# Kernel tuning notes

Measured on AMD Instinct MI355X. Metric: run time of the kernel, lower is better.

Reference implementation:

```python
import jax, jax.numpy as jnp
import numpy as np

N_NODES = 65536
N_EDGES = N_NODES * 16
NEG_SLOPE = 0.2


def setup_inputs() -> dict:
    key = jax.random.key(0)
    ks = jax.random.split(key, 32)
    x = jax.random.normal(ks[0], (N_NODES, 336), dtype=jnp.float32)
    ei = jax.random.randint(ks[1], (2, N_EDGES), 0, N_NODES)
    src, dst = ei[0], ei[1]
    dst = jnp.where(src == dst, (dst + 1) % N_NODES, dst)  # no pre-existing self-loops
    edge_index = jnp.stack([src, dst])
    batch = jnp.arange(N_NODES) // 8

    def mk(k, shape, fan_in):
        return jax.random.normal(k, shape, dtype=jnp.float32) * (1.0 / np.sqrt(fan_in))

    conv_dims = [(336, 125), (250, 75), (150, 50), (100, 30)]
    H = 2
    p = {}
    ki = 2
    for i, (cin, cout) in enumerate(conv_dims, 1):
        p[f"W{i}"] = mk(ks[ki], (cin, H * cout), cin); ki += 1
        p[f"as{i}"] = mk(ks[ki], (H, cout), cout); ki += 1
        p[f"ad{i}"] = mk(ks[ki], (H, cout), cout); ki += 1
        p[f"b{i}"] = jnp.zeros((H * cout,), dtype=jnp.float32)
    lin_dims = [(480, 200), (200, 100), (100, 100), (100, 29)]
    for i, (cin, cout) in enumerate(lin_dims, 1):
        p[f"lw{i}"] = mk(ks[ki], (cin, cout), cin); ki += 1
        p[f"lb{i}"] = jnp.zeros((cout,), dtype=jnp.float32)
    return {"x": x, "edge_index": edge_index, "batch": batch, **p}


def gat_conv(x, src, dst, W, a_src, a_dst, bias):
    # PyG GATConv (concat=True): gather -> LeakyReLU score -> segment softmax over dst -> scatter-add
    N = x.shape[0]
    H, C = a_src.shape
    h = (x @ W).reshape(N, H, C)                      # [N,H,C]
    al_s = jnp.sum(h * a_src, axis=-1)                # [N,H]
    al_d = jnp.sum(h * a_dst, axis=-1)
    e = jax.nn.leaky_relu(al_s[src] + al_d[dst], NEG_SLOPE)  # [E,H]
    m = jax.ops.segment_max(e, dst, num_segments=N)   # [N,H]
    m = jnp.where(jnp.isfinite(m), m, 0.0)
    ex = jnp.exp(e - m[dst])
    den = jax.ops.segment_sum(ex, dst, num_segments=N)
    alpha = ex / den[dst]                             # [E,H]
    out = jax.ops.segment_sum(alpha[:, :, None] * h[src], dst, num_segments=N)
    return out.reshape(N, H * C) + bias


def reference(x, edge_index, batch,
              W1, as1, ad1, b1, W2, as2, ad2, b2,
              W3, as3, ad3, b3, W4, as4, ad4, b4,
              lw1, lb1, lw2, lb2, lw3, lb3, lw4, lb4):
    N = x.shape[0]
    loops = jnp.arange(N)
    src = jnp.concatenate([edge_index[0], loops])  # add self-loops (PyG default)
    dst = jnp.concatenate([edge_index[1], loops])
    h = jax.nn.relu(gat_conv(x, src, dst, W1, as1, ad1, b1))
    h = jax.nn.relu(gat_conv(h, src, dst, W2, as2, ad2, b2))
    h = jax.nn.relu(gat_conv(h, src, dst, W3, as3, ad3, b3))
    h = jax.nn.relu(gat_conv(h, src, dst, W4, as4, ad4, b4))
    h = h.reshape(-1, 480)                         # 8 nodes per graph * 60 feats
    h = jax.nn.relu(h @ lw1 + lb1)
    h = jax.nn.relu(h @ lw2 + lb2)
    h = jax.nn.relu(h @ lw3 + lb3)
    return h @ lw4 + lb4
```

## Files before the change

### kernel.cpp

```cpp
#include <hip/hip_runtime.h>
#include <hip/hip_bf16.h>
#include <stdint.h>

#define N_NODES 65536
#define N_EDGES (N_NODES * 16)
#define NEG_SLOPE 0.2f

typedef short bf16x8 __attribute__((ext_vector_type(8)));
typedef float f32x4 __attribute__((ext_vector_type(4)));

__device__ __forceinline__ unsigned short f2bf(float f) {
    unsigned u = __float_as_uint(f);
    u += 0x7fffu + ((u >> 16) & 1u);
    return (unsigned short)(u >> 16);
}
__device__ __forceinline__ float bf2f(unsigned short h) {
    return __uint_as_float(((unsigned)h) << 16);
}
__device__ __forceinline__ void load_lds16(const void* g, void* l) {
    __builtin_amdgcn_global_load_lds(
        (const __attribute__((address_space(1))) unsigned int*)g,
        (__attribute__((address_space(3))) unsigned int*)l, 16, 0, 0);
}

template<int TN>
__global__ __launch_bounds__(256) void gemm_mfma(
    const float* __restrict__ A32, int KA,
    const unsigned short* __restrict__ Ahi, const unsigned short* __restrict__ Alo,
    int lda, int Kp,
    const unsigned short* __restrict__ Bhi, const unsigned short* __restrict__ Blo,
    const float* __restrict__ bias, int Nbias,
    float* __restrict__ C32,
    unsigned short* __restrict__ Chi, unsigned short* __restrict__ Clo,
    int ldc, int Nw, int relu,
    const float* __restrict__ asrc, const float* __restrict__ adst,
    float* __restrict__ alS, float* __restrict__ alD, int Cal, int HCal)
{
    constexpr int NI = TN / 32;
    __shared__ unsigned short sAhi[128 * 32], sAlo[128 * 32];
    __shared__ unsigned short sBhi[TN * 32],  sBlo[TN * 32];
    __shared__ float sAl[128][2][4];
    const int tid = threadIdx.x;
    const int wave = tid >> 6, lane = tid & 63;
    const int row0 = blockIdx.y * 128;
    const int col0 = blockIdx.x * TN;
    const int wm = (wave & 1) * 64, wn = (wave >> 1) * (TN / 2);
    const int mlane = lane & 15, q = lane >> 4;

    f32x4 acc[4][NI];
#pragma unroll
    for (int a = 0; a < 4; ++a)
#pragma unroll
        for (int b = 0; b < NI; ++b) acc[a][b] = (f32x4){0.f, 0.f, 0.f, 0.f};

    for (int k0 = 0; k0 < Kp; k0 += 32) {
        __syncthreads();
        if (A32) {
            const int r = tid >> 1, cbase = (tid & 1) * 16;
            const float* Ap = A32 + (size_t)(row0 + r) * lda;
#pragma unroll
            for (int j = 0; j < 4; ++j) {
                int kc = k0 + cbase + j * 4;
                float4 v = make_float4(0.f, 0.f, 0.f, 0.f);
                if (kc < KA) v = *(const float4*)(Ap + kc);
                ushort4 h, l;
                h.x = f2bf(v.x); l.x = f2bf(v.x - bf2f(h.x));
                h.y = f2bf(v.y); l.y = f2bf(v.y - bf2f(h.y));
                h.z = f2bf(v.z); l.z = f2bf(v.z - bf2f(h.z));
                h.w = f2bf(v.w); l.w = f2bf(v.w - bf2f(h.w));
                *(ushort4*)(sAhi + r * 32 + cbase + j * 4) = h;
                *(ushort4*)(sAlo + r * 32 + cbase + j * 4) = l;
            }
        } else {
#pragma unroll
            for (int cc = 0; cc < 2; ++cc) {
                int c = wave * 2 + cc;
                int r = c * 16 + (lane >> 2);
                size_t goff = (size_t)(row0 + r) * lda + k0 + (lane & 3) * 8;
                load_lds16(Ahi + goff, sAhi + c * 512);
                load_lds16(Alo + goff, sAlo + c * 512);
            }
        }
        {
#pragma unroll
            for (int cc = 0; cc < TN / 64; ++cc) {
                int c = wave * (TN / 64) + cc;
                int r = c * 16 + (lane >> 2);
                size_t goff = (size_t)(col0 + r) * Kp + k0 + (lane & 3) * 8;
                load_lds16(Bhi + goff, sBhi + c * 512);
                load_lds16(Blo + goff, sBlo + c * 512);
            }
        }
        __syncthreads();

        bf16x8 ah[4], al[4], bh[NI], bl[NI];
#pragma unroll
        for (int mi = 0; mi < 4; ++mi) {
            int m = wm + mi * 16 + mlane;
            ah[mi] = *(const bf16x8*)(sAhi + m * 32 + q * 8);
            al[mi] = *(const bf16x8*)(sAlo + m * 32 + q * 8);
        }
#pragma unroll
        for (int ni = 0; ni < NI; ++ni) {
            int n = wn + ni * 16 + mlane;
            bh[ni] = *(const bf16x8*)(sBhi + n * 32 + q * 8);
            bl[ni] = *(const bf16x8*)(sBlo + n * 32 + q * 8);
        }
#pragma unroll
        for (int mi = 0; mi < 4; ++mi)
#pragma unroll
            for (int ni = 0; ni < NI; ++ni) {
                acc[mi][ni] = __builtin_amdgcn_mfma_f32_16x16x32_bf16(ah[mi], bh[ni], acc[mi][ni], 0, 0, 0);
                acc[mi][ni] = __builtin_amdgcn_mfma_f32_16x16x32_bf16(al[mi], bh[ni], acc[mi][ni], 0, 0, 0);
                acc[mi][ni] = __builtin_amdgcn_mfma_f32_16x16x32_bf16(ah[mi], bl[ni], acc[mi][ni], 0, 0, 0);
            }
    }

#pragma unroll
    for (int ni = 0; ni < NI; ++ni) {
        int col = col0 + wn + ni * 16 + mlane;
        if (col >= Nw) continue;
        float bv = (bias && col < Nbias) ? bias[col] : 0.f;
#pragma unroll
        for (int mi = 0; mi < 4; ++mi) {
#pragma unroll
            for (int reg = 0; reg < 4; ++reg) {
                int row = row0 + wm + mi * 16 + q * 4 + reg;
                float v = acc[mi][ni][reg] + bv;
                if (relu) v = fmaxf(v, 0.f);
                size_t off = (size_t)row * ldc + col;
                if (Chi) {
                    unsigned short h = f2bf(v);
                    Chi[off] = h;
                    Clo[off] = f2bf(v - bf2f(h));
                } else {
                    C32[off] = v;
                }
            }
        }
    }

    if (asrc) {
        float asv[NI], adv[NI];
        bool head0[NI];
#pragma unroll
        for (int ni = 0; ni < NI; ++ni) {
            int col = col0 + wn + ni * 16 + mlane;
            bool valid = col < HCal;
            head0[ni] = col < Cal;
            asv[ni] = valid ? asrc[col] : 0.f;
            adv[ni] = valid ? adst[col] : 0.f;
        }
#pragma unroll
        for (int mi = 0; mi < 4; ++mi) {
#pragma unroll
            for (int reg = 0; reg < 4; ++reg) {
                float s0 = 0.f, s1 = 0.f, d0 = 0.f, d1 = 0.f;
#pragma unroll
                for (int ni = 0; ni < NI; ++ni) {
                    float v = acc[mi][ni][reg];
                    if (head0[ni]) { s0 += v * asv[ni]; d0 += v * adv[ni]; }
                    else           { s1 += v * asv[ni]; d1 += v * adv[ni]; }
                }
#pragma unroll
                for (int off = 1; off < 16; off <<= 1) {
                    s0 += __shfl_xor(s0, off); s1 += __shfl_xor(s1, off);
                    d0 += __shfl_xor(d0, off); d1 += __shfl_xor(d1, off);
                }
                if (mlane == 0) {
                    int rl = wm + mi * 16 + q * 4 + reg;
                    int slot = wave >> 1;
                    sAl[rl][slot][0] = s0; sAl[rl][slot][1] = s1;
                    sAl[rl][slot][2] = d0; sAl[rl][slot][3] = d1;
                }
            }
        }
        __syncthreads();
        if (tid < 128) {
            int row = row0 + tid;
            float v0 = sAl[tid][0][0] + sAl[tid][1][0];
            float v1 = sAl[tid][0][1] + sAl[tid][1][1];
            float v2 = sAl[tid][0][2] + sAl[tid][1][2];
            float v3 = sAl[tid][0][3] + sAl[tid][1][3];
            atomicAdd(&alS[row * 2 + 0], v0);
            atomicAdd(&alS[row * 2 + 1], v1);
            atomicAdd(&alD[row * 2 + 0], v2);
            atomicAdd(&alD[row * 2 + 1], v3);
        }
    }
}

template<int NI>
__device__ __forceinline__ void mlp_layer(
    const unsigned short* aHi, const unsigned short* aLo, int ldaS, int K,
    const unsigned short* __restrict__ Bhi, const unsigned short* __restrict__ Blo,
    int Kp,
    unsigned short* sBh, unsigned short* sBl,
    const float* __restrict__ bias, int Nbias, int colBase,
    unsigned short* oHi, unsigned short* oLo, int ldo, int Nstore,
    float* __restrict__ gOut, int row0, int relu,
    int wave, int lane)
{
    const int mlane = lane & 15, q = lane >> 4;
    const int wm = (wave & 1) * 16;
    const int wn = (wave >> 1) * (NI * 16);
    f32x4 acc[NI];
#pragma unroll
    for (int b = 0; b < NI; ++b) acc[b] = (f32x4){0.f, 0.f, 0.f, 0.f};

    for (int k0 = 0; k0 < K; k0 += 32) {
        __syncthreads();
        for (int c = wave; c < NI * 2; c += 4) {
            int r = c * 16 + (lane >> 2);
            size_t goff = (size_t)r * Kp + k0 + (lane & 3) * 8;
            load_lds16(Bhi + goff, sBh + c * 512);
            load_lds16(Blo + goff, sBl + c * 512);
        }
        __syncthreads();

        bf16x8 ah, al, bh[NI], bl[NI];
        ah = *(const bf16x8*)(aHi + (wm + mlane) * ldaS + k0 + q * 8);
        al = *(const bf16x8*)(aLo + (wm + mlane) * ldaS + k0 + q * 8);
#pragma unroll
        for (int ni = 0; ni < NI; ++ni) {
            int n = wn + ni * 16 + mlane;
            bh[ni] = *(const bf16x8*)(sBh + n * 32 + q * 8);
            bl[ni] = *(const bf16x8*)(sBl + n * 32 + q * 8);
        }
#pragma unroll
        for (int ni = 0; ni < NI; ++ni) {
            acc[ni] = __builtin_amdgcn_mfma_f32_16x16x32_bf16(ah, bh[ni], acc[ni], 0, 0, 0);
            acc[ni] = __builtin_amdgcn_mfma_f32_16x16x32_bf16(al, bh[ni], acc[ni], 0, 0, 0);
            acc[ni] = __builtin_amdgcn_mfma_f32_16x16x32_bf16(ah, bl[ni], acc[ni], 0, 0, 0);
        }
    }
    __syncthreads();

#pragma unroll
    for (int ni = 0; ni < NI; ++ni) {
        int colg = colBase + wn + ni * 16 + mlane;
        float bv = (colg < Nbias) ? bias[colg] : 0.f;
#pragma unroll
        for (int reg = 0; reg < 4; ++reg) {
            int row = wm + q * 4 + reg;
            float v = acc[ni][reg] + bv;
            if (relu) v = fmaxf(v, 0.f);
            if (gOut) {
                if (colg < 29) gOut[(size_t)(row0 + row) * 29 + colg] = v;
            } else if (colg < Nstore) {
                unsigned short h = f2bf(v);
                oHi[row * ldo + colg] = h;
                oLo[row * ldo + colg] = f2bf(v - bf2f(h));
            }
        }
    }
}

__global__ __launch_bounds__(256) void mlp_fused(
    const unsigned short* __restrict__ actHi, const unsigned short* __restrict__ actLo,
    const unsigned short* __restrict__ L1h, const unsigned short* __restrict__ L1l,
    const unsigned short* __restrict__ L2h, const unsigned short* __restrict__ L2l,
    const unsigned short* __restrict__ L3h, const unsigned short* __restrict__ L3l,
    const unsigned short* __restrict__ L4h, const unsigned short* __restrict__ L4l,
    const float* __restrict__ B1, const float* __restrict__ B2,
    const float* __restrict__ B3, const float* __restrict__ B4,
    float* __restrict__ out)
{
    __shared__ unsigned short b1h[32 * 224], b1l[32 * 224];
    __shared__ unsigned short b2h[32 * 128], b2l[32 * 128];
    __shared__ unsigned short sAh[32 * 32],  sAl[32 * 32];
    __shared__ unsigned short sBh[128 * 32], sBl[128 * 32];
    const int tid = threadIdx.x;
    const int wave = tid >> 6, lane = tid & 63;
    const int row0 = blockIdx.x * 32;
    const int mlane = lane & 15, q = lane >> 4;
    const int wm = (wave & 1) * 16;
    const int wn = (wave >> 1) * 64;

    for (int nt = 0; nt < 2; ++nt) {
        const unsigned short* Bh = L1h + (size_t)nt * 128 * 512;
        const unsigned short* Bl = L1l + (size_t)nt * 128 * 512;
        f32x4 acc[4];
#pragma unroll
        for (int b = 0; b < 4; ++b) acc[b] = (f32x4){0.f, 0.f, 0.f, 0.f};
        for (int k0 = 0; k0 < 512; k0 += 32) {
            __syncthreads();
            for (int c = wave; c < 2; c += 4) {
                int r = c * 16 + (lane >> 2);
                size_t goff = (size_t)(row0 + r) * 512 + k0 + (lane & 3) * 8;
                load_lds16(actHi + goff, sAh + c * 512);
                load_lds16(actLo + goff, sAl + c * 512);
            }
            for (int c = wave; c < 8; c += 4) {
                int r = c * 16 + (lane >> 2);
                size_t goff = (size_t)r * 512 + k0 + (lane & 3) * 8;
                load_lds16(Bh + goff, sBh + c * 512);
                load_lds16(Bl + goff, sBl + c * 512);
            }
            __syncthreads();
            bf16x8 ah = *(const bf16x8*)(sAh + (wm + mlane) * 32 + q * 8);
            bf16x8 al = *(const bf16x8*)(sAl + (wm + mlane) * 32 + q * 8);
#pragma unroll
            for (int ni = 0; ni < 4; ++ni) {
                int n = wn + ni * 16 + mlane;
                bf16x8 bh = *(const bf16x8*)(sBh + n * 32 + q * 8);
                bf16x8 bl = *(const bf16x8*)(sBl + n * 32 + q * 8);
                acc[ni] = __builtin_amdgcn_mfma_f32_16x16x32_bf16(ah, bh, acc[ni], 0, 0, 0);
                acc[ni] = __builtin_amdgcn_mfma_f32_16x16x32_bf16(al, bh, acc[ni], 0, 0, 0);
                acc[ni] = __builtin_amdgcn_mfma_f32_16x16x32_bf16(ah, bl, acc[ni], 0, 0, 0);
            }
        }
        __syncthreads();
#pragma unroll
        for (int ni = 0; ni < 4; ++ni) {
            int colg = nt * 128 + wn + ni * 16 + mlane;
            float bv = (colg < 200) ? B1[colg] : 0.f;
#pragma unroll
            for (int reg = 0; reg < 4; ++reg) {
                int row = wm + q * 4 + reg;
                float v = fmaxf(acc[ni][reg] + bv, 0.f);
                if (colg < 224) {
                    unsigned short h = f2bf(v);
                    b1h[row * 224 + colg] = h;
                    b1l[row * 224 + colg] = f2bf(v - bf2f(h));
                }
            }
        }
    }
    __syncthreads();

    mlp_layer<4>(b1h, b1l, 224, 224, L2h, L2l, 224, sBh, sBl,
                 B2, 100, 0, b2h, b2l, 128, 128, nullptr, 0, 1, wave, lane);
    __syncthreads();
    mlp_layer<4>(b2h, b2l, 128, 128, L3h, L3l, 128, sBh, sBl,
                 B3, 100, 0, b1h, b1l, 128, 128, nullptr, 0, 1, wave, lane);
    __syncthreads();
    mlp_layer<2>(b1h, b1l, 128, 128, L4h, L4l, 128, sBh, sBl,
                 B4, 29, 0, nullptr, nullptr, 0, 0, out, row0, 0, wave, lane);
}

struct WtJob {
    const float* W; unsigned short* Whi; unsigned short* Wlo;
    int K, N, Kp, remap, nb0;
};
struct WtJobs { WtJob j[8]; };

__global__ void wt_decomp_all(WtJobs jobs)
{
    int b = blockIdx.x;
    int idx = 0;
#pragma unroll
    for (int i = 1; i < 8; ++i)
        if (b >= jobs.j[i].nb0) idx = i;
    WtJob jb = jobs.j[idx];
    int n = b - jb.nb0;
    for (int k = threadIdx.x; k < jb.Kp; k += 256) {
        int ks = k, valid = 1;
        if (jb.remap) {
            int bb = k >> 6, r = k & 63;
            if (r < 60) ks = bb * 60 + r; else valid = 0;
        }
        float v = 0.f;
        if (valid && ks < jb.K && n < jb.N) v = jb.W[(size_t)ks * jb.N + n];
        unsigned short h = f2bf(v);
        jb.Whi[(size_t)n * jb.Kp + k] = h;
        jb.Wlo[(size_t)n * jb.Kp + k] = f2bf(v - bf2f(h));
    }
}

template<int LPE>
__global__ __launch_bounds__(256) void gat_gather_fused(
    const float* __restrict__ hlin,
    const float* __restrict__ al_s, const float* __restrict__ al_d,
    const int* __restrict__ indptr, const int* __restrict__ csr_src,
    const float* __restrict__ bias,
    unsigned short* __restrict__ outHi, unsigned short* __restrict__ outLo,
    int ldo, int Nn, int C, int HC, int HCpad)
{
    constexpr int G = 64 / LPE;
    const int wave = threadIdx.x >> 6, lane = threadIdx.x & 63;
    const int i = blockIdx.x * 4 + wave;
    if (i >= Nn) return;
    const int start = indptr[i], end = indptr[i + 1];
    const float ad0 = al_d[2 * i], ad1 = al_d[2 * i + 1];

    float m0 = -1e30f, m1 = -1e30f, den0 = 0.f, den1 = 0.f;
    for (int j = start + lane; j < end; j += 64) {
        int s = csr_src[j];
        float2 as = *(const float2*)(al_s + 2 * s);
        float e0 = as.x + ad0; e0 = e0 > 0.f ? e0 : NEG_SLOPE * e0;
        float e1 = as.y + ad1; e1 = e1 > 0.f ? e1 : NEG_SLOPE * e1;
        float n0 = fmaxf(m0, e0);
        den0 = den0 * __expf(m0 - n0) + __expf(e0 - n0);
        m0 = n0;
        float n1 = fmaxf(m1, e1);
        den1 = den1 * __expf(m1 - n1) + __expf(e1 - n1);
        m1 = n1;
    }
#pragma unroll
    for (int off = 32; off; off >>= 1) {
        float mo0 = __shfl_xor(m0, off), do0 = __shfl_xor(den0, off);
        float n0 = fmaxf(m0, mo0);
        den0 = den0 * __expf(m0 - n0) + do0 * __expf(mo0 - n0);
        m0 = n0;
        float mo1 = __shfl_xor(m1, off), do1 = __shfl_xor(den1, off);
        float n1 = fmaxf(m1, mo1);
        den1 = den1 * __expf(m1 - n1) + do1 * __expf(mo1 - n1);
        m1 = n1;
    }
    const float inv0 = 1.f / den0, inv1 = 1.f / den1;

    const int l = lane % LPE;
    const int g = lane / LPE;
    const int ch4 = l * 4;
    const bool chA = ch4 < HCpad;
    float a0 = 0.f, a1 = 0.f, a2 = 0.f, a3 = 0.f;
    const bool h0 = (ch4 + 0) < C, h1 = (ch4 + 1) < C,
               h2 = (ch4 + 2) < C, h3 = (ch4 + 3) < C;

    for (int jb = start; jb < end; jb += 4 * G) {
#pragma unroll
        for (int u = 0; u < 4; ++u) {
            int j = jb + u * G + g;
            int jj = j < end ? j : end - 1;
            int s = csr_src[jj];
            float2 as = *(const float2*)(al_s + 2 * s);
            float e0 = as.x + ad0; e0 = e0 > 0.f ? e0 : NEG_SLOPE * e0;
            float e1 = as.y + ad1; e1 = e1 > 0.f ? e1 : NEG_SLOPE * e1;
            float w0 = __expf(e0 - m0) * inv0;
            float w1 = __expf(e1 - m1) * inv1;
            if (j >= end) { w0 = 0.f; w1 = 0.f; }
            const float* hr = hlin + (size_t)s * HCpad;
            float4 h = chA ? *(const float4*)(hr + ch4)
                           : make_float4(0.f, 0.f, 0.f, 0.f);
            a0 = fmaf(h0 ? w0 : w1, h.x, a0);
            a1 = fmaf(h1 ? w0 : w1, h.y, a1);
            a2 = fmaf(h2 ? w0 : w1, h.z, a2);
            a3 = fmaf(h3 ? w0 : w1, h.w, a3);
        }
    }
#pragma unroll
    for (int off = LPE; off < 64; off <<= 1) {
        a0 += __shfl_xor(a0, off);
        a1 += __shfl_xor(a1, off);
        a2 += __shfl_xor(a2, off);
        a3 += __shfl_xor(a3, off);
    }
    if (g == 0 && chA) {
        float bx = (ch4 + 0 < HC) ? bias[ch4 + 0] : 0.f;
        float by = (ch4 + 1 < HC) ? bias[ch4 + 1] : 0.f;
        float bz = (ch4 + 2 < HC) ? bias[ch4 + 2] : 0.f;
        float bw = (ch4 + 3 < HC) ? bias[ch4 + 3] : 0.f;
        float v0 = fmaxf(a0 + bx, 0.f);
        float v1 = fmaxf(a1 + by, 0.f);
        float v2 = fmaxf(a2 + bz, 0.f);
        float v3 = fmaxf(a3 + bw, 0.f);
        ushort4 h, lo;
        h.x = f2bf(v0); lo.x = f2bf(v0 - bf2f(h.x));
        h.y = f2bf(v1); lo.y = f2bf(v1 - bf2f(h.y));
        h.z = f2bf(v2); lo.z = f2bf(v2 - bf2f(h.z));
        h.w = f2bf(v3); lo.w = f2bf(v3 - bf2f(h.w));
        *(ushort4*)(outHi + (size_t)i * ldo + ch4) = h;
        *(ushort4*)(outLo + (size_t)i * ldo + ch4) = lo;
    }
    for (int z = HCpad + lane * 4; z < ldo; z += 256) {
        ushort4 zz; zz.x = zz.y = zz.z = zz.w = 0;
        *(ushort4*)(outHi + (size_t)i * ldo + z) = zz;
        *(ushort4*)(outLo + (size_t)i * ldo + z) = zz;
    }
}

__global__ void hist_self_k(const int* __restrict__ dst, int E,
                            int* __restrict__ counts, int n)
{
    int gid = blockIdx.x * blockDim.x + threadIdx.x;
    if (gid < E) atomicAdd(&counts[dst[gid]], 1);
    else if (gid < E + n) atomicAdd(&counts[gid - E], 1);
}

__global__ void scan_block_k(const int* __restrict__ in, int* __restrict__ out,
                             int* __restrict__ bsum, int n)
{
    __shared__ int sh[256];
    int gid = blockIdx.x * 256 + threadIdx.x;
    int v = (gid < n) ? in[gid] : 0;
    sh[threadIdx.x] = v;
    __syncthreads();
    for (int off = 1; off < 256; off <<= 1) {
        int t = (threadIdx.x >= off) ? sh[threadIdx.x - off] : 0;
        __syncthreads();
        sh[threadIdx.x] += t;
        __syncthreads();
    }
    int incl = sh[threadIdx.x];
    if (gid < n) out[gid] = incl - v;
    if (threadIdx.x == 255) bsum[blockIdx.x] = incl;
}

__global__ void scan_tops_k(const int* __restrict__ bsum, int* __restrict__ boff)
{
    __shared__ int sh[256];
    int v = bsum[threadIdx.x];
    sh[threadIdx.x] = v;
    __syncthreads();
    for (int off = 1; off < 256; off <<= 1) {
        int t = (threadIdx.x >= off) ? sh[threadIdx.x - off] : 0;
        __syncthreads();
        sh[threadIdx.x] += t;
        __syncthreads();
    }
    boff[threadIdx.x] = sh[threadIdx.x] - v;
}

__global__ void scan_add_k(int* __restrict__ indptr, const int* __restrict__ boff,
                           int n, int Etot)
{
    int gid = blockIdx.x * 256 + threadIdx.x;
    if (gid < n) indptr[gid] += boff[blockIdx.x];
    if (gid == 0) indptr[n] = Etot;
}

__global__ void fill_all_k(const int* __restrict__ src, const int* __restrict__ dst,
                           int E, const int* __restrict__ indptr,
                           int* __restrict__ cursor, int* __restrict__ csr_src, int n)
{
    int gid = blockIdx.x * blockDim.x + threadIdx.x;
    if (gid < E) {
        int d = dst[gid];
        int pos = atomicAdd(&cursor[d], 1);
        csr_src[indptr[d] + pos] = src[gid];
    } else if (gid < E + n) {
        int i = gid - E;
        int pos = atomicAdd(&cursor[i], 1);
        csr_src[indptr[i] + pos] = i;
    }
}

extern "C" void kernel_launch(void* const* d_in, const int* in_sizes, int n_in,
                              void* d_out, int out_size, void* d_ws, size_t ws_size,
                              hipStream_t stream)
{
    (void)in_sizes; (void)n_in; (void)out_size; (void)ws_size;
    const int N = N_NODES;
    const int E = N_EDGES;
    const int Etot = E + N;

    const float* x = (const float*)d_in[0];
    const int* ei = (const int*)d_in[1];
    const float* Wc[4] = {(const float*)d_in[3], (const float*)d_in[7],
                          (const float*)d_in[11], (const float*)d_in[15]};
    const float* AS[4] = {(const float*)d_in[4], (const float*)d_in[8],
                          (const float*)d_in[12], (const float*)d_in[16]};
    const float* AD[4] = {(const float*)d_in[5], (const float*)d_in[9],
                          (const float*)d_in[13], (const float*)d_in[17]};
    const float* Bc[4] = {(const float*)d_in[6], (const float*)d_in[10],
                          (const float*)d_in[14], (const float*)d_in[18]};
    const float* LW[4] = {(const float*)d_in[19], (const float*)d_in[21],
                          (const float*)d_in[23], (const float*)d_in[25]};
    const float* LB[4] = {(const float*)d_in[20], (const float*)d_in[22],
                          (const float*)d_in[24], (const float*)d_in[26]};

    char* w = (char*)d_ws;
    auto alloc = [&](size_t bytes) -> char* {
        char* p = w; w += (bytes + 255) & ~(size_t)255; return p;
    };
    float* bufC = (float*)alloc((size_t)N * 256 * 4);
    unsigned short* actHi = (unsigned short*)alloc((size_t)N * 256 * 2);
    unsigned short* actLo = (unsigned short*)alloc((size_t)N * 256 * 2);
    int* csr    = (int*)alloc((size_t)Etot * 4);
    float* alSD = (float*)alloc((size_t)N * 4 * 4 * 4 + (size_t)N * 2 * 4);
    int* cnt2   = (int*)(alSD + (size_t)N * 16);
    int* counts = cnt2;
    int* cursor = cnt2 + N;
    int* indptr = (int*)alloc((size_t)(N + 8) * 4);
    int* bsum   = (int*)alloc(1024);
    int* boff   = (int*)alloc(1024);

    const int KpConv[4] = {352, 256, 160, 128};
    const int NpConv[4] = {256, 192, 128, 64};
    const int KpLin[4]  = {512, 224, 128, 128};
    const int NpLin[4]  = {256, 128, 128, 64};
    unsigned short *WtHi[4], *WtLo[4], *LtHi[4], *LtLo[4];
    for (int l = 0; l < 4; ++l) {
        WtHi[l] = (unsigned short*)alloc((size_t)NpConv[l] * KpConv[l] * 2);
        WtLo[l] = (unsigned short*)alloc((size_t)NpConv[l] * KpConv[l] * 2);
    }
    for (int l = 0; l < 4; ++l) {
        LtHi[l] = (unsigned short*)alloc((size_t)NpLin[l] * KpLin[l] * 2);
        LtLo[l] = (unsigned short*)alloc((size_t)NpLin[l] * KpLin[l] * 2);
    }

    const int* esrc = ei;
    const int* edst = ei + E;

    hipMemsetAsync(alSD, 0, (size_t)N * 4 * 4 * 4 + (size_t)N * 2 * 4, stream);
    hist_self_k<<<(E + N) / 256, 256, 0, stream>>>(edst, E, counts, N);
    scan_block_k<<<N / 256, 256, 0, stream>>>(counts, indptr, bsum, N);
    scan_tops_k<<<1, 256, 0, stream>>>(bsum, boff);
    scan_add_k<<<N / 256, 256, 0, stream>>>(indptr, boff, N, Etot);
    fill_all_k<<<(E + N) / 256, 256, 0, stream>>>(esrc, edst, E, indptr, cursor, csr, N);

    const int Kc[4] = {336, 250, 150, 100}, Nc[4] = {250, 150, 100, 60};
    const int Kl[4] = {480, 200, 100, 100}, Nl[4] = {200, 100, 100, 29};
    WtJobs jobs;
    int nb = 0;
    for (int l = 0; l < 4; ++l) {
        jobs.j[l] = {Wc[l], WtHi[l], WtLo[l], Kc[l], Nc[l], KpConv[l], 0, nb};
        nb += NpConv[l];
    }
    for (int l = 0; l < 4; ++l) {
        jobs.j[4 + l] = {LW[l], LtHi[l], LtLo[l], Kl[l], Nl[l], KpLin[l],
                         l == 0 ? 1 : 0, nb};
        nb += NpLin[l];
    }
    wt_decomp_all<<<nb, 256, 0, stream>>>(jobs);

    const int HCp[4]  = {256, 152, 100, 60};
    const int ldoA[4] = {256, 160, 128, 64};
    const int ldaA[4] = {336, 256, 160, 128};
    for (int l = 0; l < 4; ++l) {
        int C = Nc[l] / 2, HC = Nc[l];
        float* alS = alSD + (size_t)l * N * 4;
        float* alD = alS + (size_t)N * 2;
        if (l == 0) {
            gemm_mfma<128><<<dim3(2, N / 128), 256, 0, stream>>>(
                x, 336, nullptr, nullptr, 336, 352,
                WtHi[0], WtLo[0], nullptr, 0,
                bufC, nullptr, nullptr, HCp[0], HCp[0], 0,
                AS[0], AD[0], alS, alD, C, HC);
        } else if (l == 1) {
            gemm_mfma<64><<<dim3(3, N / 128), 256, 0, stream>>>(
                nullptr, 0, actHi, actLo, ldaA[1], KpConv[1],
                WtHi[1], WtLo[1], nullptr, 0,
                bufC, nullptr, nullptr, HCp[1], HCp[1], 0,
                AS[1], AD[1], alS, alD, C, HC);
        } else if (l == 2) {
            gemm_mfma<128><<<dim3(1, N / 128), 256, 0, stream>>>(
                nullptr, 0, actHi, actLo, ldaA[2], KpConv[2],
                WtHi[2], WtLo[2], nullptr, 0,
                bufC, nullptr, nullptr, HCp[2], HCp[2], 0,
                AS[2], AD[2], alS, alD, C, HC);
        } else {
            gemm_mfma<64><<<dim3(1, N / 128), 256, 0, stream>>>(
                nullptr, 0, actHi, actLo, ldaA[3], KpConv[3],
                WtHi[3], WtLo[3], nullptr, 0,
                bufC, nullptr, nullptr, HCp[3], HCp[3], 0,
                AS[3], AD[3], alS, alD, C, HC);
        }
        if (l == 0) {
            gat_gather_fused<64><<<N / 4, 256, 0, stream>>>(
                bufC, alS, alD, indptr, csr, Bc[0],
                actHi, actLo, ldoA[0], N, C, HC, HCp[0]);
        } else if (l == 1) {
            gat_gather_fused<64><<<N / 4, 256, 0, stream>>>(
                bufC, alS, alD, indptr, csr, Bc[1],
                actHi, actLo, ldoA[1], N, C, HC, HCp[1]);
        } else if (l == 2) {
            gat_gather_fused<32><<<N / 4, 256, 0, stream>>>(
                bufC, alS, alD, indptr, csr, Bc[2],
                actHi, actLo, ldoA[2], N, C, HC, HCp[2]);
        } else {
            gat_gather_fused<16><<<N / 4, 256, 0, stream>>>(
                bufC, alS, alD, indptr, csr, Bc[3],
                actHi, actLo, ldoA[3], N, C, HC, HCp[3]);
        }
    }

    mlp_fused<<<8192 / 32, 256, 0, stream>>>(
        actHi, actLo,
        LtHi[0], LtLo[0], LtHi[1], LtLo[1],
        LtHi[2], LtLo[2], LtHi[3], LtLo[3],
        LB[0], LB[1], LB[2], LB[3],
        (float*)d_out);
}
```

Before: 951.5 us.

## Split layer-1 GAT gather into softmax stats pass and channel-sliced gather

Layer 1's fused gather is replaced by two kernels. The first computes the per-node softmax max and inverse denominator. The second assigns each lane 4 channels of one node, and the grid is ordered by channel slice so that feature columns of the source rows stay cache-resident across neighbouring blocks. CSR source indices are narrowed to 16-bit, which halves index traffic and only works because N is 65536. Output stores become nontemporal. The cost is an extra kernel and recomputing the edge scores in both passes.

```diff
diff --git a/kernel.cpp b/kernel.cpp
--- a/kernel.cpp
+++ b/kernel.cpp
@@ -5,9 +5,11 @@
 #define N_NODES 65536
 #define N_EDGES (N_NODES * 16)
 #define NEG_SLOPE 0.2f
+#define NB_L1 (N_NODES / 64)
 
 typedef short bf16x8 __attribute__((ext_vector_type(8)));
 typedef float f32x4 __attribute__((ext_vector_type(4)));
+typedef unsigned int u32x2 __attribute__((ext_vector_type(2)));
 
 __device__ __forceinline__ unsigned short f2bf(float f) {
     unsigned u = __float_as_uint(f);
@@ -21,6 +23,12 @@
     __builtin_amdgcn_global_load_lds(
         (const __attribute__((address_space(1))) unsigned int*)g,
         (__attribute__((address_space(3))) unsigned int*)l, 16, 0, 0);
+}
+__device__ __forceinline__ void nt_store_us4(unsigned short* p, ushort4 v) {
+    u32x2 d;
+    d.x = (unsigned)v.x | ((unsigned)v.y << 16);
+    d.y = (unsigned)v.z | ((unsigned)v.w << 16);
+    __builtin_nontemporal_store(d, (u32x2*)p);
 }
 
 template<int TN>
@@ -368,11 +376,117 @@
     }
 }
 
+__global__ __launch_bounds__(256) void attn_stats(
+    const float* __restrict__ al_s, const float* __restrict__ al_d,
+    const int* __restrict__ indptr, const unsigned short* __restrict__ csr_src,
+    float4* __restrict__ stats, int Nn)
+{
+    const int wave = threadIdx.x >> 6, lane = threadIdx.x & 63;
+    const int i = blockIdx.x * 4 + wave;
+    if (i >= Nn) return;
+    const int start = indptr[i], end = indptr[i + 1];
+    const float ad0 = al_d[2 * i], ad1 = al_d[2 * i + 1];
+
+    float m0 = -1e30f, m1 = -1e30f, den0 = 0.f, den1 = 0.f;
+    for (int j = start + lane; j < end; j += 64) {
+        int s = csr_src[j];
+        float2 as = *(const float2*)(al_s + 2 * s);
+        float e0 = as.x + ad0; e0 = e0 > 0.f ? e0 : NEG_SLOPE * e0;
+        float e1 = as.y + ad1; e1 = e1 > 0.f ? e1 : NEG_SLOPE * e1;
+        float n0 = fmaxf(m0, e0);
+        den0 = den0 * __expf(m0 - n0) + __expf(e0 - n0);
+        m0 = n0;
+        float n1 = fmaxf(m1, e1);
+        den1 = den1 * __expf(m1 - n1) + __expf(e1 - n1);
+        m1 = n1;
+    }
+#pragma unroll
+    for (int off = 32; off; off >>= 1) {
+        float mo0 = __shfl_xor(m0, off), do0 = __shfl_xor(den0, off);
+        float n0 = fmaxf(m0, mo0);
+        den0 = den0 * __expf(m0 - n0) + do0 * __expf(mo0 - n0);
+        m0 = n0;
+        float mo1 = __shfl_xor(m1, off), do1 = __shfl_xor(den1, off);
+        float n1 = fmaxf(m1, mo1);
+        den1 = den1 * __expf(m1 - n1) + do1 * __expf(mo1 - n1);
+        m1 = n1;
+    }
+    if (lane == 0) {
+        float4 st;
+        st.x = m0; st.y = m1;
+        st.z = 1.f / den0; st.w = 1.f / den1;
+        stats[i] = st;
+    }
+}
+
+__global__ __launch_bounds__(256) void gat_gather_slice(
+    const float* __restrict__ hlin,
+    const float* __restrict__ al_s, const float* __restrict__ al_d,
+    const float4* __restrict__ stats,
+    const int* __restrict__ indptr, const unsigned short* __restrict__ csr_src,
+    const float* __restrict__ bias,
+    unsigned short* __restrict__ outHi, unsigned short* __restrict__ outLo,
+    int C, int HC)
+{
+    const int bid = blockIdx.x;
+    const int s8 = bid & 7;
+    const int rest = bid >> 3;
+    const int nb = rest & (NB_L1 - 1);
+    const int phase = rest / NB_L1;
+    const int slice = phase * 8 + s8;
+
+    const int lane = threadIdx.x & 63;
+    const int wave = threadIdx.x >> 6;
+    const int l = lane & 3;
+    const int nd = lane >> 2;
+    const int i = nb * 64 + wave * 16 + nd;
+    const int ch = slice * 16 + l * 4;
+
+    const int start = indptr[i], end = indptr[i + 1];
+    const float ad0 = al_d[2 * i], ad1 = al_d[2 * i + 1];
+    const float4 st = stats[i];
+    const float m0 = st.x, m1 = st.y, inv0 = st.z, inv1 = st.w;
+    const bool h0 = (ch + 0) < C, h1 = (ch + 1) < C,
+               h2 = (ch + 2) < C, h3 = (ch + 3) < C;
+
+    float a0 = 0.f, a1 = 0.f, a2 = 0.f, a3 = 0.f;
+    const float* hbase = hlin + ch;
+    for (int j = start; j < end; ++j) {
+        int s = __builtin_nontemporal_load(csr_src + j);
+        float2 as = *(const float2*)(al_s + 2 * s);
+        float e0 = as.x + ad0; e0 = e0 > 0.f ? e0 : NEG_SLOPE * e0;
+        float e1 = as.y + ad1; e1 = e1 > 0.f ? e1 : NEG_SLOPE * e1;
+        float w0 = __expf(e0 - m0) * inv0;
+        float w1 = __expf(e1 - m1) * inv1;
+        float4 h = *(const float4*)(hbase + (size_t)s * 256);
+        a0 = fmaf(h0 ? w0 : w1, h.x, a0);
+        a1 = fmaf(h1 ? w0 : w1, h.y, a1);
+        a2 = fmaf(h2 ? w0 : w1, h.z, a2);
+        a3 = fmaf(h3 ? w0 : w1, h.w, a3);
+    }
+
+    float bx = (ch + 0 < HC) ? bias[ch + 0] : 0.f;
+    float by = (ch + 1 < HC) ? bias[ch + 1] : 0.f;
+    float bz = (ch + 2 < HC) ? bias[ch + 2] : 0.f;
+    float bw = (ch + 3 < HC) ? bias[ch + 3] : 0.f;
+    float v0 = fmaxf(a0 + bx, 0.f);
+    float v1 = fmaxf(a1 + by, 0.f);
+    float v2 = fmaxf(a2 + bz, 0.f);
+    float v3 = fmaxf(a3 + bw, 0.f);
+    ushort4 h, lo;
+    h.x = f2bf(v0); lo.x = f2bf(v0 - bf2f(h.x));
+    h.y = f2bf(v1); lo.y = f2bf(v1 - bf2f(h.y));
+    h.z = f2bf(v2); lo.z = f2bf(v2 - bf2f(h.z));
+    h.w = f2bf(v3); lo.w = f2bf(v3 - bf2f(h.w));
+    nt_store_us4(outHi + (size_t)i * 256 + ch, h);
+    nt_store_us4(outLo + (size_t)i * 256 + ch, lo);
+}
+
 template<int LPE>
 __global__ __launch_bounds__(256) void gat_gather_fused(
     const float* __restrict__ hlin,
     const float* __restrict__ al_s, const float* __restrict__ al_d,
-    const int* __restrict__ indptr, const int* __restrict__ csr_src,
+    const int* __restrict__ indptr, const unsigned short* __restrict__ csr_src,
     const float* __restrict__ bias,
     unsigned short* __restrict__ outHi, unsigned short* __restrict__ outLo,
     int ldo, int Nn, int C, int HC, int HCpad)
@@ -460,8 +574,8 @@
         h.y = f2bf(v1); lo.y = f2bf(v1 - bf2f(h.y));
         h.z = f2bf(v2); lo.z = f2bf(v2 - bf2f(h.z));
         h.w = f2bf(v3); lo.w = f2bf(v3 - bf2f(h.w));
-        *(ushort4*)(outHi + (size_t)i * ldo + ch4) = h;
-        *(ushort4*)(outLo + (size_t)i * ldo + ch4) = lo;
+        nt_store_us4(outHi + (size_t)i * ldo + ch4, h);
+        nt_store_us4(outLo + (size_t)i * ldo + ch4, lo);
     }
     for (int z = HCpad + lane * 4; z < ldo; z += 256) {
         ushort4 zz; zz.x = zz.y = zz.z = zz.w = 0;
@@ -522,17 +636,18 @@
 
 __global__ void fill_all_k(const int* __restrict__ src, const int* __restrict__ dst,
                            int E, const int* __restrict__ indptr,
-                           int* __restrict__ cursor, int* __restrict__ csr_src, int n)
+                           int* __restrict__ cursor,
+                           unsigned short* __restrict__ csr_src, int n)
 {
     int gid = blockIdx.x * blockDim.x + threadIdx.x;
     if (gid < E) {
         int d = dst[gid];
         int pos = atomicAdd(&cursor[d], 1);
-        csr_src[indptr[d] + pos] = src[gid];
+        csr_src[indptr[d] + pos] = (unsigned short)src[gid];
     } else if (gid < E + n) {
         int i = gid - E;
         int pos = atomicAdd(&cursor[i], 1);
-        csr_src[indptr[i] + pos] = i;
+        csr_src[indptr[i] + pos] = (unsigned short)i;
     }
 }
 
@@ -567,7 +682,8 @@
     float* bufC = (float*)alloc((size_t)N * 256 * 4);
     unsigned short* actHi = (unsigned short*)alloc((size_t)N * 256 * 2);
     unsigned short* actLo = (unsigned short*)alloc((size_t)N * 256 * 2);
-    int* csr    = (int*)alloc((size_t)Etot * 4);
+    unsigned short* csr = (unsigned short*)alloc((size_t)Etot * 2);
+    float4* stats = (float4*)alloc((size_t)N * 16);
     float* alSD = (float*)alloc((size_t)N * 4 * 4 * 4 + (size_t)N * 2 * 4);
     int* cnt2   = (int*)(alSD + (size_t)N * 16);
     int* counts = cnt2;
@@ -648,9 +764,10 @@
                 AS[3], AD[3], alS, alD, C, HC);
         }
         if (l == 0) {
-            gat_gather_fused<64><<<N / 4, 256, 0, stream>>>(
-                bufC, alS, alD, indptr, csr, Bc[0],
-                actHi, actLo, ldoA[0], N, C, HC, HCp[0]);
+            attn_stats<<<N / 4, 256, 0, stream>>>(alS, alD, indptr, csr, stats, N);
+            gat_gather_slice<<<2 * 8 * NB_L1, 256, 0, stream>>>(
+                bufC, alS, alD, stats, indptr, csr, Bc[0],
+                actHi, actLo, C, HC);
         } else if (l == 1) {
             gat_gather_fused<64><<<N / 4, 256, 0, stream>>>(
                 bufC, alS, alD, indptr, csr, Bc[1],
```

New measurement: 1.290 ms. 35.6% more time.
